# Optimization experiments

Measured on AMD Instinct MI355X. Metric: run time of the kernel, lower is better.

## Reference

```python
import jax, jax.numpy as jnp
import numpy as np

N, F_IN, E = 50000, 128, 800000
HID, HEADS, EMB = 32, 8, 64
NEG_SLOPE = 0.2


def gat_conv(x, src, dst, W_src, W_dst, att_src, att_dst, bias, heads, out_ch, concat):
    n = x.shape[0]
    h_src = (x @ W_src).reshape(n, heads, out_ch)   # [N,H,C]
    h_dst = (x @ W_dst).reshape(n, heads, out_ch)
    a_src = jnp.sum(h_src * att_src, axis=-1)       # [N,H]
    a_dst = jnp.sum(h_dst * att_dst, axis=-1)
    e = jax.nn.leaky_relu(a_src[src] + a_dst[dst], NEG_SLOPE)  # [E,H]
    # segment softmax over destination nodes (stable, max detached as in PyG)
    m = jax.ops.segment_max(e, dst, num_segments=n)
    m = jnp.where(jnp.isfinite(m), m, 0.0)
    ex = jnp.exp(e - jax.lax.stop_gradient(m)[dst])
    denom = jax.ops.segment_sum(ex, dst, num_segments=n)
    alpha = ex / (denom[dst] + 1e-16)               # [E,H]
    msg = h_src[src] * alpha[:, :, None]            # [E,H,C]
    out = jax.ops.segment_sum(msg, dst, num_segments=n)  # [N,H,C]
    if concat:
        out = out.reshape(n, heads * out_ch)
    else:
        out = out.mean(axis=1)
    return out + bias


def setup_inputs() -> dict:
    key = jax.random.key(0)
    ks = jax.random.split(key, 12)
    g = lambda k, shape: jax.random.normal(k, shape, dtype=jnp.float32) * (1.0 / np.sqrt(shape[0]))
    x = jax.random.normal(ks[0], (N, F_IN), dtype=jnp.float32)
    edge_index = jax.random.randint(ks[1], (2, E), 0, N, dtype=jnp.int64)
    return {
        "x": x,
        "edge_index": edge_index,
        "W_src1": g(ks[2], (F_IN, HEADS * HID)),
        "W_dst1": g(ks[3], (F_IN, HEADS * HID)),
        "att_src1": g(ks[4], (HEADS, HID)) * 0.1,
        "att_dst1": g(ks[5], (HEADS, HID)) * 0.1,
        "b1": jnp.zeros((HEADS * HID,), dtype=jnp.float32),
        "W_src2": g(ks[6], (HEADS * HID, EMB)),
        "W_dst2": g(ks[7], (HEADS * HID, EMB)),
        "att_src2": g(ks[8], (1, EMB)) * 0.1,
        "att_dst2": g(ks[9], (1, EMB)) * 0.1,
        "b2": jnp.zeros((EMB,), dtype=jnp.float32),
    }


def reference(x, edge_index, W_src1, W_dst1, att_src1, att_dst1, b1,
              W_src2, W_dst2, att_src2, att_dst2, b2):
    src, dst = edge_index[0], edge_index[1]
    h = gat_conv(x, src, dst, W_src1, W_dst1, att_src1, att_dst1, b1, HEADS, HID, True)
    h = jax.nn.relu(h)
    out = gat_conv(h, src, dst, W_src2, W_dst2, att_src2, att_dst2, b2, 1, EMB, False)
    return out
```

## Files before the change

kernel.cpp:

```cpp
#include <hip/hip_runtime.h>
#include <hip/hip_bf16.h>
#include <cstdint>
#include <cstddef>

#define NN    50000
#define FIN   128
#define EE    800000
#define HID_  32
#define HEADS_ 8
#define EMB_  64
#define NEG   0.2f
#define NB_SCAN 196
#define LOG2E 1.4426950408889634f

typedef short bf16x8 __attribute__((ext_vector_type(8)));
typedef float f32x4  __attribute__((ext_vector_type(4)));

static __device__ __forceinline__ ushort f2bf(float f){
    uint u = __float_as_uint(f);
    uint r = (u + 0x7FFFu + ((u >> 16) & 1u)) >> 16;
    return (ushort)r;
}
static __device__ __forceinline__ float bf2f(ushort u){
    return __uint_as_float(((uint)u) << 16);
}
static __device__ __forceinline__ float pexp(float t){
    return __builtin_amdgcn_exp2f(fmaxf(t, NEG * t));
}

__global__ __launch_bounds__(256) void k_prep(const float* __restrict__ Wsrc1, const float* __restrict__ Wdst1,
                                              const float* __restrict__ asrc1, const float* __restrict__ adst1,
                                              const float* __restrict__ Wsrc2, const float* __restrict__ Wdst2,
                                              const float* __restrict__ asrc2, const float* __restrict__ adst2,
                                              ushort* __restrict__ wt1bf, float* __restrict__ wt2,
                                              ushort* __restrict__ w1t, ushort* __restrict__ w2t){
    int idx = blockIdx.x * blockDim.x + threadIdx.x;
    if (idx < 2048){
        int f = idx >> 4, j = idx & 15;
        const float* W; const float* a; int h;
        if (j < 8) { W = Wsrc1; a = asrc1; h = j; } else { W = Wdst1; a = adst1; h = j - 8; }
        float s = 0.f;
        #pragma unroll
        for (int c = 0; c < HID_; ++c)
            s += W[(size_t)f * (HEADS_ * HID_) + h * HID_ + c] * a[h * HID_ + c];
        wt1bf[j * 128 + f] = f2bf(s * LOG2E);
    } else if (idx < 2560){
        int t = idx - 2048;
        int f = t >> 1, j = t & 1;
        const float* W = j ? Wdst2 : Wsrc2;
        const float* a = j ? adst2 : asrc2;
        float s = 0.f;
        #pragma unroll
        for (int c = 0; c < EMB_; ++c) s += W[(size_t)f * EMB_ + c] * a[c];
        wt2[j * 256 + f] = s * LOG2E;
    } else if (idx < 35328){
        int t = idx - 2560;
        int n = t >> 7, k = t & 127;
        w1t[t] = f2bf(Wsrc1[(size_t)k * 256 + n]);
    } else if (idx < 51712){
        int t = idx - 35328;
        int n = t >> 8, k = t & 255;
        w2t[t] = f2bf(Wsrc2[(size_t)k * 64 + n]);
    }
}

__global__ void k_hist(const int* __restrict__ dst, int* __restrict__ deg, int* __restrict__ rank){
    int e = blockIdx.x * blockDim.x + threadIdx.x;
    if (e < EE) rank[e] = atomicAdd(&deg[dst[e]], 1);
}

__global__ __launch_bounds__(256) void k_scanall(const int* __restrict__ deg, int* __restrict__ row_ptr,
                                                 int* __restrict__ bsum, int* __restrict__ flags){
    __shared__ int s[256];
    __shared__ int ps[256];
    int tid = threadIdx.x, b = blockIdx.x;
    int i = b * 256 + tid;
    int v = (i < NN) ? deg[i] : 0;
    s[tid] = v;
    __syncthreads();
    #pragma unroll
    for (int off = 1; off < 256; off <<= 1){
        int t = (tid >= off) ? s[tid - off] : 0;
        __syncthreads();
        s[tid] += t;
        __syncthreads();
    }
    if (tid == 255){
        bsum[b] = s[255];
        __hip_atomic_store(&flags[b], 1, __ATOMIC_RELEASE, __HIP_MEMORY_SCOPE_AGENT);
    }
    int p = 0;
    if (tid < b){
        while (__hip_atomic_load(&flags[tid], __ATOMIC_ACQUIRE, __HIP_MEMORY_SCOPE_AGENT) == 0){}
        p = bsum[tid];
    }
    ps[tid] = p;
    __syncthreads();
    #pragma unroll
    for (int off = 128; off > 0; off >>= 1){
        if (tid < off) ps[tid] += ps[tid + off];
        __syncthreads();
    }
    int boff = ps[0];
    if (i < NN) row_ptr[i] = boff + s[tid] - v;
    if (b == 0 && tid == 0) row_ptr[NN] = EE;
}

__global__ void k_scatter(const int* __restrict__ src, const int* __restrict__ dst,
                          const int* __restrict__ row_ptr, const int* __restrict__ rank,
                          int* __restrict__ col){
    int e = blockIdx.x * blockDim.x + threadIdx.x;
    if (e < EE){
        int d = dst[e];
        col[row_ptr[d] + rank[e]] = src[e];
    }
}

__global__ __launch_bounds__(256) void k_gemm1_mfma(const float* __restrict__ x,
                                                    const ushort* __restrict__ w1t,
                                                    const ushort* __restrict__ wt1bf,
                                                    ushort* __restrict__ c,
                                                    float* __restrict__ a_src1,
                                                    float* __restrict__ a_dst1){
    __shared__ ushort As[64][136];
    __shared__ ushort Bs[128][136];
    __shared__ ushort Bsa[16][136];
    const int tid = threadIdx.x;
    const int m0 = blockIdx.x * 64;
    const int n0 = blockIdx.y * 128;
    #pragma unroll
    for (int i = 0; i < 8; ++i){
        int idx = tid + i * 256;
        int r = idx >> 5, c4 = idx & 31;
        int m = m0 + r;
        float4 v = make_float4(0.f, 0.f, 0.f, 0.f);
        if (m < NN) v = *(const float4*)&x[(size_t)m * FIN + c4 * 4];
        ushort4 u; u.x = f2bf(v.x); u.y = f2bf(v.y); u.z = f2bf(v.z); u.w = f2bf(v.w);
        *(ushort4*)&As[r][c4 * 4] = u;
    }
    #pragma unroll
    for (int i = 0; i < 8; ++i){
        int idx = tid + i * 256;
        int r = idx >> 4, c8 = idx & 15;
        const ushort4* s4 = (const ushort4*)&w1t[(size_t)(n0 + r) * 128 + c8 * 8];
        *(ushort4*)&Bs[r][c8 * 8]     = s4[0];
        *(ushort4*)&Bs[r][c8 * 8 + 4] = s4[1];
    }
    if (blockIdx.y == 0){
        int r = tid >> 4, c8 = tid & 15;
        const ushort4* s4 = (const ushort4*)&wt1bf[r * 128 + c8 * 8];
        *(ushort4*)&Bsa[r][c8 * 8]     = s4[0];
        *(ushort4*)&Bsa[r][c8 * 8 + 4] = s4[1];
    }
    __syncthreads();
    const int lane = tid & 63;
    const int w    = tid >> 6;
    const int mr   = lane & 15;
    const int kg   = lane >> 4;
    f32x4 acc[8];
    #pragma unroll
    for (int i = 0; i < 8; ++i) acc[i] = (f32x4){0.f, 0.f, 0.f, 0.f};
    f32x4 acca = (f32x4){0.f, 0.f, 0.f, 0.f};
    #pragma unroll
    for (int ks = 0; ks < 4; ++ks){
        bf16x8 a = *(const bf16x8*)&As[w * 16 + mr][ks * 32 + kg * 8];
        #pragma unroll
        for (int nf = 0; nf < 8; ++nf){
            bf16x8 b = *(const bf16x8*)&Bs[nf * 16 + mr][ks * 32 + kg * 8];
            acc[nf] = __builtin_amdgcn_mfma_f32_16x16x32_bf16(a, b, acc[nf], 0, 0, 0);
        }
        if (blockIdx.y == 0){
            bf16x8 ba = *(const bf16x8*)&Bsa[mr][ks * 32 + kg * 8];
            acca = __builtin_amdgcn_mfma_f32_16x16x32_bf16(a, ba, acca, 0, 0, 0);
        }
    }
    #pragma unroll
    for (int nf = 0; nf < 8; ++nf){
        int colb = n0 + nf * 16 + mr;
        #pragma unroll
        for (int r = 0; r < 4; ++r){
            int row = m0 + w * 16 + kg * 4 + r;
            if (row < NN) c[(size_t)row * 256 + colb] = f2bf(acc[nf][r]);
        }
    }
    if (blockIdx.y == 0){
        int j = mr;
        #pragma unroll
        for (int r = 0; r < 4; ++r){
            int row = m0 + w * 16 + kg * 4 + r;
            if (row < NN){
                if (j < 8) a_src1[(size_t)row * 8 + j]       = acca[r];
                else       a_dst1[(size_t)row * 8 + (j - 8)] = acca[r];
            }
        }
    }
}

__global__ __launch_bounds__(256) void k_gemm2_mfma(const ushort* __restrict__ hbf,
                                                    const ushort* __restrict__ w2t,
                                                    ushort* __restrict__ c2){
    __shared__ ushort As[64][264];
    __shared__ ushort Bs[64][264];
    const int tid = threadIdx.x;
    const int m0 = blockIdx.x * 64;
    #pragma unroll
    for (int i = 0; i < 8; ++i){
        int idx = tid + i * 256;
        int r = idx >> 5, c8 = idx & 31;
        int m = m0 + r;
        ushort4 v0 = make_ushort4(0,0,0,0), v1 = make_ushort4(0,0,0,0);
        if (m < NN){
            const ushort4* s4 = (const ushort4*)&hbf[(size_t)m * 256 + c8 * 8];
            v0 = s4[0]; v1 = s4[1];
        }
        *(ushort4*)&As[r][c8 * 8]     = v0;
        *(ushort4*)&As[r][c8 * 8 + 4] = v1;
    }
    #pragma unroll
    for (int i = 0; i < 8; ++i){
        int idx = tid + i * 256;
        int r = idx >> 5, c8 = idx & 31;
        const ushort4* s4 = (const ushort4*)&w2t[(size_t)r * 256 + c8 * 8];
        *(ushort4*)&Bs[r][c8 * 8]     = s4[0];
        *(ushort4*)&Bs[r][c8 * 8 + 4] = s4[1];
    }
    __syncthreads();
    const int lane = tid & 63;
    const int w    = tid >> 6;
    const int mr   = lane & 15;
    const int kg   = lane >> 4;
    f32x4 acc[4];
    #pragma unroll
    for (int i = 0; i < 4; ++i) acc[i] = (f32x4){0.f, 0.f, 0.f, 0.f};
    #pragma unroll
    for (int ks = 0; ks < 8; ++ks){
        bf16x8 a = *(const bf16x8*)&As[w * 16 + mr][ks * 32 + kg * 8];
        #pragma unroll
        for (int nf = 0; nf < 4; ++nf){
            bf16x8 b = *(const bf16x8*)&Bs[nf * 16 + mr][ks * 32 + kg * 8];
            acc[nf] = __builtin_amdgcn_mfma_f32_16x16x32_bf16(a, b, acc[nf], 0, 0, 0);
        }
    }
    #pragma unroll
    for (int nf = 0; nf < 4; ++nf){
        int colb = nf * 16 + mr;
        #pragma unroll
        for (int r = 0; r < 4; ++r){
            int row = m0 + w * 16 + kg * 4 + r;
            if (row < NN) c2[(size_t)row * 64 + colb] = f2bf(acc[nf][r]);
        }
    }
}

__global__ __launch_bounds__(256) void k_agg1(const ushort* __restrict__ hsrc, const float* __restrict__ a_src,
                                              const float* __restrict__ a_dst, const int* __restrict__ row_ptr,
                                              const int* __restrict__ col, const float* __restrict__ b1,
                                              const float* __restrict__ wt2,
                                              ushort* __restrict__ hout_bf,
                                              float* __restrict__ a_src2, float* __restrict__ a_dst2){
    int node = blockIdx.x * 4 + (threadIdx.x >> 6);
    if (node >= NN) return;
    int lane = threadIdx.x & 63;
    int head = lane >> 3;
    float ad = a_dst[(size_t)node * 8 + head];
    const ushort4* h4 = (const ushort4*)hsrc;
    float4 acc = make_float4(0.f, 0.f, 0.f, 0.f);
    float den = 0.f;
    int b = row_ptr[node], en = row_ptr[node + 1];
    int i = b;
    for (; i + 8 <= en; i += 8){
        int ss[8]; float e[8]; ushort4 v[8]; float p[8];
        #pragma unroll
        for (int j = 0; j < 8; ++j) ss[j] = col[i + j];
        #pragma unroll
        for (int j = 0; j < 8; ++j) e[j] = a_src[(size_t)ss[j] * 8 + head];
        #pragma unroll
        for (int j = 0; j < 8; ++j) v[j] = h4[(size_t)ss[j] * 64 + lane];
        #pragma unroll
        for (int j = 0; j < 8; ++j) p[j] = pexp(e[j] + ad);
        #pragma unroll
        for (int j = 0; j < 8; ++j){
            acc.x += p[j] * bf2f(v[j].x);
            acc.y += p[j] * bf2f(v[j].y);
            acc.z += p[j] * bf2f(v[j].z);
            acc.w += p[j] * bf2f(v[j].w);
            den += p[j];
        }
    }
    for (; i < en; ++i){
        int s = col[i];
        float p = pexp(a_src[(size_t)s * 8 + head] + ad);
        ushort4 v = h4[(size_t)s * 64 + lane];
        acc.x += p * bf2f(v.x); acc.y += p * bf2f(v.y);
        acc.z += p * bf2f(v.z); acc.w += p * bf2f(v.w);
        den += p;
    }
    float inv = 1.f / (den + 1e-16f);
    float4 bb = ((const float4*)b1)[lane];
    float4 o;
    o.x = fmaxf(acc.x * inv + bb.x, 0.f);
    o.y = fmaxf(acc.y * inv + bb.y, 0.f);
    o.z = fmaxf(acc.z * inv + bb.z, 0.f);
    o.w = fmaxf(acc.w * inv + bb.w, 0.f);
    ushort4 ob; ob.x = f2bf(o.x); ob.y = f2bf(o.y); ob.z = f2bf(o.z); ob.w = f2bf(o.w);
    ((ushort4*)hout_bf)[(size_t)node * 64 + lane] = ob;
    float4 ws4 = ((const float4*)wt2)[lane];
    float4 wd4 = ((const float4*)(wt2 + 256))[lane];
    float ss2 = o.x*ws4.x + o.y*ws4.y + o.z*ws4.z + o.w*ws4.w;
    float sd2 = o.x*wd4.x + o.y*wd4.y + o.z*wd4.z + o.w*wd4.w;
    #pragma unroll
    for (int off = 32; off > 0; off >>= 1){
        ss2 += __shfl_xor(ss2, off);
        sd2 += __shfl_xor(sd2, off);
    }
    if (lane == 0){ a_src2[node] = ss2; a_dst2[node] = sd2; }
}

__global__ __launch_bounds__(256) void k_agg2(const ushort* __restrict__ h2bf, const float* __restrict__ a_src2,
                                              const float* __restrict__ a_dst2, const int* __restrict__ row_ptr,
                                              const int* __restrict__ col, const float* __restrict__ b2,
                                              float* __restrict__ out){
    int node = blockIdx.x * 4 + (threadIdx.x >> 6);
    if (node >= NN) return;
    int lane = threadIdx.x & 63;
    float ad = a_dst2[node];
    float acc = 0.f, den = 0.f;
    int b = row_ptr[node], en = row_ptr[node + 1];
    int i = b;
    for (; i + 8 <= en; i += 8){
        int ss[8]; float e[8]; ushort u[8]; float p[8];
        #pragma unroll
        for (int j = 0; j < 8; ++j) ss[j] = col[i + j];
        #pragma unroll
        for (int j = 0; j < 8; ++j) e[j] = a_src2[ss[j]];
        #pragma unroll
        for (int j = 0; j < 8; ++j) u[j] = h2bf[(size_t)ss[j] * 64 + lane];
        #pragma unroll
        for (int j = 0; j < 8; ++j) p[j] = pexp(e[j] + ad);
        #pragma unroll
        for (int j = 0; j < 8; ++j){
            acc += p[j] * bf2f(u[j]);
            den += p[j];
        }
    }
    for (; i < en; ++i){
        int s = col[i];
        float p = pexp(a_src2[s] + ad);
        acc += p * bf2f(h2bf[(size_t)s * 64 + lane]);
        den += p;
    }
    out[(size_t)node * 64 + lane] = acc / (den + 1e-16f) + b2[lane];
}

extern "C" void kernel_launch(void* const* d_in, const int* in_sizes, int n_in,
                              void* d_out, int out_size, void* d_ws, size_t ws_size,
                              hipStream_t stream){
    const float* x        = (const float*)d_in[0];
    const int*   ei       = (const int*)  d_in[1];
    const float* Wsrc1    = (const float*)d_in[2];
    const float* Wdst1    = (const float*)d_in[3];
    const float* att_src1 = (const float*)d_in[4];
    const float* att_dst1 = (const float*)d_in[5];
    const float* b1       = (const float*)d_in[6];
    const float* Wsrc2    = (const float*)d_in[7];
    const float* Wdst2    = (const float*)d_in[8];
    const float* att_src2 = (const float*)d_in[9];
    const float* att_dst2 = (const float*)d_in[10];
    const float* b2       = (const float*)d_in[11];
    float* out = (float*)d_out;
    const int* srcp = ei;
    const int* dstp = ei + EE;

    char* base = (char*)d_ws;
    ushort* hbf1   = (ushort*)base;  base += (size_t)NN * 256 * 2;
    ushort* hrel   = (ushort*)base;  base += (size_t)NN * 256 * 2;
    ushort* h2bf   = (ushort*)base;  base += (size_t)NN * 64 * 2;
    float*  a_src1 = (float*)base;   base += (size_t)NN * 8 * 4;
    float*  a_dst1 = (float*)base;   base += (size_t)NN * 8 * 4;
    float*  a_src2 = (float*)base;   base += (size_t)NN * 4;
    float*  a_dst2 = (float*)base;   base += (size_t)NN * 4;
    ushort* wt1bf  = (ushort*)base;  base += 2048 * 2;
    float*  wt2    = (float*)base;   base += 512 * 4;
    ushort* w1t    = (ushort*)base;  base += 32768 * 2;
    ushort* w2t    = (ushort*)base;  base += 16384 * 2;
    int* deg     = (int*)base;       base += (size_t)NN * 4;
    int* flags   = (int*)base;       base += 256 * 4;
    int* row_ptr = (int*)base;       base += (size_t)(NN + 1) * 4;
    int* rank    = (int*)base;       base += (size_t)EE * 4;
    int* col     = (int*)base;       base += (size_t)EE * 4;
    int* bsum    = (int*)base;       base += 256 * 4;

    hipMemsetAsync(deg, 0, (NN + 256) * sizeof(int), stream);

    k_prep<<<202, 256, 0, stream>>>(Wsrc1, Wdst1, att_src1, att_dst1,
                                    Wsrc2, Wdst2, att_src2, att_dst2,
                                    wt1bf, wt2, w1t, w2t);

    k_hist<<<(EE + 255) / 256, 256, 0, stream>>>(dstp, deg, rank);
    k_scanall<<<NB_SCAN, 256, 0, stream>>>(deg, row_ptr, bsum, flags);
    k_scatter<<<(EE + 255) / 256, 256, 0, stream>>>(srcp, dstp, row_ptr, rank, col);

    dim3 g1((NN + 63) / 64, 2);
    k_gemm1_mfma<<<g1, 256, 0, stream>>>(x, w1t, wt1bf, hbf1, a_src1, a_dst1);

    k_agg1<<<(NN + 3) / 4, 256, 0, stream>>>(hbf1, a_src1, a_dst1, row_ptr, col, b1, wt2,
                                             hrel, a_src2, a_dst2);

    k_gemm2_mfma<<<(NN + 63) / 64, 256, 0, stream>>>(hrel, w2t, h2bf);

    k_agg2<<<(NN + 3) / 4, 256, 0, stream>>>(h2bf, a_src2, a_dst2, row_ptr, col, b2, out);
}
```

Before: 217.2 us.

## Split node features into per-head 32-channel planes for cache-local gathers

Stores layer-1 and layer-2 features as head-major planes of 32 bf16 channels per node. The aggregation kernels become head-sliced: each block handles one plane, with four edges processed in parallel per wavefront and combined by shuffles. The second-layer attention scalars are accumulated atomically across heads and zeroed by an extended memset. The aim is to keep each plane's gather working set small enough for cache reuse, in exchange for eight times as many blocks, repeated row_ptr and col reads per head, and float atomics.

```diff
diff --git a/kernel.cpp b/kernel.cpp
--- a/kernel.cpp
+++ b/kernel.cpp
@@ -180,7 +180,8 @@
         #pragma unroll
         for (int r = 0; r < 4; ++r){
             int row = m0 + w * 16 + kg * 4 + r;
-            if (row < NN) c[(size_t)row * 256 + colb] = f2bf(acc[nf][r]);
+            if (row < NN)
+                c[((size_t)(colb >> 5) * NN + row) * 32 + (colb & 31)] = f2bf(acc[nf][r]);
         }
     }
     if (blockIdx.y == 0){
@@ -210,7 +211,7 @@
         int m = m0 + r;
         ushort4 v0 = make_ushort4(0,0,0,0), v1 = make_ushort4(0,0,0,0);
         if (m < NN){
-            const ushort4* s4 = (const ushort4*)&hbf[(size_t)m * 256 + c8 * 8];
+            const ushort4* s4 = (const ushort4*)&hbf[((size_t)(c8 >> 2) * NN + m) * 32 + (c8 & 3) * 8];
             v0 = s4[0]; v1 = s4[1];
         }
         *(ushort4*)&As[r][c8 * 8]     = v0;
@@ -247,109 +248,123 @@
         #pragma unroll
         for (int r = 0; r < 4; ++r){
             int row = m0 + w * 16 + kg * 4 + r;
-            if (row < NN) c2[(size_t)row * 64 + colb] = f2bf(acc[nf][r]);
-        }
-    }
-}
-
-__global__ __launch_bounds__(256) void k_agg1(const ushort* __restrict__ hsrc, const float* __restrict__ a_src,
-                                              const float* __restrict__ a_dst, const int* __restrict__ row_ptr,
-                                              const int* __restrict__ col, const float* __restrict__ b1,
-                                              const float* __restrict__ wt2,
-                                              ushort* __restrict__ hout_bf,
-                                              float* __restrict__ a_src2, float* __restrict__ a_dst2){
-    int node = blockIdx.x * 4 + (threadIdx.x >> 6);
+            if (row < NN)
+                c2[((size_t)(colb >> 5) * NN + row) * 32 + (colb & 31)] = f2bf(acc[nf][r]);
+        }
+    }
+}
+
+__global__ __launch_bounds__(256) void k_agg1_s(const ushort* __restrict__ hb1s,
+                                                const float* __restrict__ a_src, const float* __restrict__ a_dst,
+                                                const int* __restrict__ row_ptr, const int* __restrict__ col,
+                                                const float* __restrict__ b1, const float* __restrict__ wt2,
+                                                ushort* __restrict__ hrels,
+                                                float* __restrict__ a_src2, float* __restrict__ a_dst2){
+    const int p = blockIdx.x & 7;
+    const int node = (blockIdx.x >> 3) * 4 + (threadIdx.x >> 6);
     if (node >= NN) return;
-    int lane = threadIdx.x & 63;
-    int head = lane >> 3;
-    float ad = a_dst[(size_t)node * 8 + head];
-    const ushort4* h4 = (const ushort4*)hsrc;
-    float4 acc = make_float4(0.f, 0.f, 0.f, 0.f);
-    float den = 0.f;
-    int b = row_ptr[node], en = row_ptr[node + 1];
+    const int lane = threadIdx.x & 63;
+    const int slot = lane >> 4;
+    const int c2 = lane & 15;
+    const ushort* hp = hb1s + (size_t)p * NN * 32;
+    const float ad = a_dst[(size_t)node * 8 + p];
+    float acc0 = 0.f, acc1 = 0.f, den = 0.f;
+    const int b = row_ptr[node], en = row_ptr[node + 1];
     int i = b;
     for (; i + 8 <= en; i += 8){
-        int ss[8]; float e[8]; ushort4 v[8]; float p[8];
-        #pragma unroll
-        for (int j = 0; j < 8; ++j) ss[j] = col[i + j];
-        #pragma unroll
-        for (int j = 0; j < 8; ++j) e[j] = a_src[(size_t)ss[j] * 8 + head];
-        #pragma unroll
-        for (int j = 0; j < 8; ++j) v[j] = h4[(size_t)ss[j] * 64 + lane];
-        #pragma unroll
-        for (int j = 0; j < 8; ++j) p[j] = pexp(e[j] + ad);
-        #pragma unroll
-        for (int j = 0; j < 8; ++j){
-            acc.x += p[j] * bf2f(v[j].x);
-            acc.y += p[j] * bf2f(v[j].y);
-            acc.z += p[j] * bf2f(v[j].z);
-            acc.w += p[j] * bf2f(v[j].w);
-            den += p[j];
-        }
-    }
-    for (; i < en; ++i){
-        int s = col[i];
-        float p = pexp(a_src[(size_t)s * 8 + head] + ad);
-        ushort4 v = h4[(size_t)s * 64 + lane];
-        acc.x += p * bf2f(v.x); acc.y += p * bf2f(v.y);
-        acc.z += p * bf2f(v.z); acc.w += p * bf2f(v.w);
-        den += p;
-    }
+        int iA = i + slot, iB = i + 4 + slot;
+        int sA = col[iA], sB = col[iB];
+        float eA = a_src[(size_t)sA * 8 + p];
+        float eB = a_src[(size_t)sB * 8 + p];
+        uint uA = *(const uint*)&hp[(size_t)sA * 32 + c2 * 2];
+        uint uB = *(const uint*)&hp[(size_t)sB * 32 + c2 * 2];
+        float pA = pexp(eA + ad), pB = pexp(eB + ad);
+        acc0 += pA * bf2f((ushort)(uA & 0xffff)) + pB * bf2f((ushort)(uB & 0xffff));
+        acc1 += pA * bf2f((ushort)(uA >> 16))    + pB * bf2f((ushort)(uB >> 16));
+        den  += pA + pB;
+    }
+    for (; i < en; i += 4){
+        int idx = i + slot;
+        int s = col[idx < en ? idx : en - 1];
+        float e = a_src[(size_t)s * 8 + p];
+        uint u = *(const uint*)&hp[(size_t)s * 32 + c2 * 2];
+        float pv = (idx < en) ? pexp(e + ad) : 0.f;
+        acc0 += pv * bf2f((ushort)(u & 0xffff));
+        acc1 += pv * bf2f((ushort)(u >> 16));
+        den  += pv;
+    }
+    acc0 += __shfl_xor(acc0, 16); acc0 += __shfl_xor(acc0, 32);
+    acc1 += __shfl_xor(acc1, 16); acc1 += __shfl_xor(acc1, 32);
+    den  += __shfl_xor(den , 16); den  += __shfl_xor(den , 32);
     float inv = 1.f / (den + 1e-16f);
-    float4 bb = ((const float4*)b1)[lane];
-    float4 o;
-    o.x = fmaxf(acc.x * inv + bb.x, 0.f);
-    o.y = fmaxf(acc.y * inv + bb.y, 0.f);
-    o.z = fmaxf(acc.z * inv + bb.z, 0.f);
-    o.w = fmaxf(acc.w * inv + bb.w, 0.f);
-    ushort4 ob; ob.x = f2bf(o.x); ob.y = f2bf(o.y); ob.z = f2bf(o.z); ob.w = f2bf(o.w);
-    ((ushort4*)hout_bf)[(size_t)node * 64 + lane] = ob;
-    float4 ws4 = ((const float4*)wt2)[lane];
-    float4 wd4 = ((const float4*)(wt2 + 256))[lane];
-    float ss2 = o.x*ws4.x + o.y*ws4.y + o.z*ws4.z + o.w*ws4.w;
-    float sd2 = o.x*wd4.x + o.y*wd4.y + o.z*wd4.z + o.w*wd4.w;
-    #pragma unroll
-    for (int off = 32; off > 0; off >>= 1){
-        ss2 += __shfl_xor(ss2, off);
-        sd2 += __shfl_xor(sd2, off);
-    }
-    if (lane == 0){ a_src2[node] = ss2; a_dst2[node] = sd2; }
-}
-
-__global__ __launch_bounds__(256) void k_agg2(const ushort* __restrict__ h2bf, const float* __restrict__ a_src2,
-                                              const float* __restrict__ a_dst2, const int* __restrict__ row_ptr,
-                                              const int* __restrict__ col, const float* __restrict__ b2,
-                                              float* __restrict__ out){
-    int node = blockIdx.x * 4 + (threadIdx.x >> 6);
+    int ch = p * 32 + c2 * 2;
+    float o0 = fmaxf(acc0 * inv + b1[ch],     0.f);
+    float o1 = fmaxf(acc1 * inv + b1[ch + 1], 0.f);
+    float ps = o0 * wt2[ch]       + o1 * wt2[ch + 1];
+    float pd = o0 * wt2[256 + ch] + o1 * wt2[256 + ch + 1];
+    #pragma unroll
+    for (int off = 1; off < 16; off <<= 1){
+        ps += __shfl_xor(ps, off);
+        pd += __shfl_xor(pd, off);
+    }
+    if (lane == 0){
+        atomicAdd(&a_src2[node], ps);
+        atomicAdd(&a_dst2[node], pd);
+    }
+    if (lane < 16){
+        ushort2 ob; ob.x = f2bf(o0); ob.y = f2bf(o1);
+        *(ushort2*)&hrels[((size_t)p * NN + node) * 32 + c2 * 2] = ob;
+    }
+}
+
+__global__ __launch_bounds__(256) void k_agg2_s(const ushort* __restrict__ h2s,
+                                                const float* __restrict__ a_src2, const float* __restrict__ a_dst2,
+                                                const int* __restrict__ row_ptr, const int* __restrict__ col,
+                                                const float* __restrict__ b2, float* __restrict__ out){
+    const int q = blockIdx.x & 7;
+    const int p = q >> 2;
+    const int node = ((blockIdx.x >> 3) * 4 + (q & 3)) * 4 + (threadIdx.x >> 6);
     if (node >= NN) return;
-    int lane = threadIdx.x & 63;
-    float ad = a_dst2[node];
-    float acc = 0.f, den = 0.f;
-    int b = row_ptr[node], en = row_ptr[node + 1];
+    const int lane = threadIdx.x & 63;
+    const int slot = lane >> 4;
+    const int c2 = lane & 15;
+    const ushort* hp = h2s + (size_t)p * NN * 32;
+    const float ad = a_dst2[node];
+    float acc0 = 0.f, acc1 = 0.f, den = 0.f;
+    const int b = row_ptr[node], en = row_ptr[node + 1];
     int i = b;
     for (; i + 8 <= en; i += 8){
-        int ss[8]; float e[8]; ushort u[8]; float p[8];
-        #pragma unroll
-        for (int j = 0; j < 8; ++j) ss[j] = col[i + j];
-        #pragma unroll
-        for (int j = 0; j < 8; ++j) e[j] = a_src2[ss[j]];
-        #pragma unroll
-        for (int j = 0; j < 8; ++j) u[j] = h2bf[(size_t)ss[j] * 64 + lane];
-        #pragma unroll
-        for (int j = 0; j < 8; ++j) p[j] = pexp(e[j] + ad);
-        #pragma unroll
-        for (int j = 0; j < 8; ++j){
-            acc += p[j] * bf2f(u[j]);
-            den += p[j];
-        }
-    }
-    for (; i < en; ++i){
-        int s = col[i];
-        float p = pexp(a_src2[s] + ad);
-        acc += p * bf2f(h2bf[(size_t)s * 64 + lane]);
-        den += p;
-    }
-    out[(size_t)node * 64 + lane] = acc / (den + 1e-16f) + b2[lane];
+        int iA = i + slot, iB = i + 4 + slot;
+        int sA = col[iA], sB = col[iB];
+        float eA = a_src2[sA], eB = a_src2[sB];
+        uint uA = *(const uint*)&hp[(size_t)sA * 32 + c2 * 2];
+        uint uB = *(const uint*)&hp[(size_t)sB * 32 + c2 * 2];
+        float pA = pexp(eA + ad), pB = pexp(eB + ad);
+        acc0 += pA * bf2f((ushort)(uA & 0xffff)) + pB * bf2f((ushort)(uB & 0xffff));
+        acc1 += pA * bf2f((ushort)(uA >> 16))    + pB * bf2f((ushort)(uB >> 16));
+        den  += pA + pB;
+    }
+    for (; i < en; i += 4){
+        int idx = i + slot;
+        int s = col[idx < en ? idx : en - 1];
+        float e = a_src2[s];
+        uint u = *(const uint*)&hp[(size_t)s * 32 + c2 * 2];
+        float pv = (idx < en) ? pexp(e + ad) : 0.f;
+        acc0 += pv * bf2f((ushort)(u & 0xffff));
+        acc1 += pv * bf2f((ushort)(u >> 16));
+        den  += pv;
+    }
+    acc0 += __shfl_xor(acc0, 16); acc0 += __shfl_xor(acc0, 32);
+    acc1 += __shfl_xor(acc1, 16); acc1 += __shfl_xor(acc1, 32);
+    den  += __shfl_xor(den , 16); den  += __shfl_xor(den , 32);
+    float inv = 1.f / (den + 1e-16f);
+    if (lane < 16){
+        int ch = p * 32 + c2 * 2;
+        float2 o;
+        o.x = acc0 * inv + b2[ch];
+        o.y = acc1 * inv + b2[ch + 1];
+        *(float2*)&out[(size_t)node * 64 + ch] = o;
+    }
 }
 
 extern "C" void kernel_launch(void* const* d_in, const int* in_sizes, int n_in,
@@ -372,25 +387,25 @@
     const int* dstp = ei + EE;
 
     char* base = (char*)d_ws;
-    ushort* hbf1   = (ushort*)base;  base += (size_t)NN * 256 * 2;
-    ushort* hrel   = (ushort*)base;  base += (size_t)NN * 256 * 2;
-    ushort* h2bf   = (ushort*)base;  base += (size_t)NN * 64 * 2;
+    ushort* hb1s   = (ushort*)base;  base += (size_t)NN * 256 * 2;
+    ushort* hrels  = (ushort*)base;  base += (size_t)NN * 256 * 2;
+    ushort* h2s    = (ushort*)base;  base += (size_t)NN * 64 * 2;
     float*  a_src1 = (float*)base;   base += (size_t)NN * 8 * 4;
     float*  a_dst1 = (float*)base;   base += (size_t)NN * 8 * 4;
-    float*  a_src2 = (float*)base;   base += (size_t)NN * 4;
-    float*  a_dst2 = (float*)base;   base += (size_t)NN * 4;
     ushort* wt1bf  = (ushort*)base;  base += 2048 * 2;
     float*  wt2    = (float*)base;   base += 512 * 4;
     ushort* w1t    = (ushort*)base;  base += 32768 * 2;
     ushort* w2t    = (ushort*)base;  base += 16384 * 2;
-    int* deg     = (int*)base;       base += (size_t)NN * 4;
-    int* flags   = (int*)base;       base += 256 * 4;
+    int*   deg     = (int*)base;     base += (size_t)NN * 4;
+    int*   flags   = (int*)base;     base += 256 * 4;
+    float* a_src2  = (float*)base;   base += (size_t)NN * 4;
+    float* a_dst2  = (float*)base;   base += (size_t)NN * 4;
     int* row_ptr = (int*)base;       base += (size_t)(NN + 1) * 4;
     int* rank    = (int*)base;       base += (size_t)EE * 4;
     int* col     = (int*)base;       base += (size_t)EE * 4;
     int* bsum    = (int*)base;       base += 256 * 4;
 
-    hipMemsetAsync(deg, 0, (NN + 256) * sizeof(int), stream);
+    (void)hipMemsetAsync(deg, 0, (size_t)(NN + 256 + 2 * NN) * sizeof(int), stream);
 
     k_prep<<<202, 256, 0, stream>>>(Wsrc1, Wdst1, att_src1, att_dst1,
                                     Wsrc2, Wdst2, att_src2, att_dst2,
@@ -401,12 +416,12 @@
     k_scatter<<<(EE + 255) / 256, 256, 0, stream>>>(srcp, dstp, row_ptr, rank, col);
 
     dim3 g1((NN + 63) / 64, 2);
-    k_gemm1_mfma<<<g1, 256, 0, stream>>>(x, w1t, wt1bf, hbf1, a_src1, a_dst1);
-
-    k_agg1<<<(NN + 3) / 4, 256, 0, stream>>>(hbf1, a_src1, a_dst1, row_ptr, col, b1, wt2,
-                                             hrel, a_src2, a_dst2);
-
-    k_gemm2_mfma<<<(NN + 63) / 64, 256, 0, stream>>>(hrel, w2t, h2bf);
-
-    k_agg2<<<(NN + 3) / 4, 256, 0, stream>>>(h2bf, a_src2, a_dst2, row_ptr, col, b2, out);
-}
+    k_gemm1_mfma<<<g1, 256, 0, stream>>>(x, w1t, wt1bf, hb1s, a_src1, a_dst1);
+
+    k_agg1_s<<<12500 * 8, 256, 0, stream>>>(hb1s, a_src1, a_dst1, row_ptr, col, b1, wt2,
+                                            hrels, a_src2, a_dst2);
+
+    k_gemm2_mfma<<<(NN + 63) / 64, 256, 0, stream>>>(hrels, w2t, h2s);
+
+    k_agg2_s<<<3125 * 8, 256, 0, stream>>>(h2s, a_src2, a_dst2, row_ptr, col, b2, out);
+}
```

New measurement: 354.1 us. +63.0%, slower.

## Merge prep with histogram and GEMM1 with CSR scatter; shrink aggregation unroll

Applied to the files above, without the earlier changes.

Independent kernels are merged by block-index partitioning: weight prep and the degree histogram share one launch, and the CSR scatter runs as extra blocks of the first GEMM kernel. This removes two launches and lets independent work overlap on the device. The aggregation loops also drop from an 8-edge to a 4-edge unroll with tree-summed partial products, which lowers register pressure but leaves fewer loads in flight per wave. The GEMM grid is flattened to 1D.

```diff
diff --git a/kernel.cpp b/kernel.cpp
--- a/kernel.cpp
+++ b/kernel.cpp
@@ -11,6 +11,9 @@
 #define EMB_  64
 #define NEG   0.2f
 #define NB_SCAN 196
+#define NB_PREP 202
+#define NB_EDGE 3125
+#define NB_GEMM1 1564
 #define LOG2E 1.4426950408889634f
 
 typedef short bf16x8 __attribute__((ext_vector_type(8)));
@@ -28,12 +31,19 @@
     return __builtin_amdgcn_exp2f(fmaxf(t, NEG * t));
 }
 
-__global__ __launch_bounds__(256) void k_prep(const float* __restrict__ Wsrc1, const float* __restrict__ Wdst1,
-                                              const float* __restrict__ asrc1, const float* __restrict__ adst1,
-                                              const float* __restrict__ Wsrc2, const float* __restrict__ Wdst2,
-                                              const float* __restrict__ asrc2, const float* __restrict__ adst2,
-                                              ushort* __restrict__ wt1bf, float* __restrict__ wt2,
-                                              ushort* __restrict__ w1t, ushort* __restrict__ w2t){
+__global__ __launch_bounds__(256) void k_prep_hist(const float* __restrict__ Wsrc1, const float* __restrict__ Wdst1,
+                                                   const float* __restrict__ asrc1, const float* __restrict__ adst1,
+                                                   const float* __restrict__ Wsrc2, const float* __restrict__ Wdst2,
+                                                   const float* __restrict__ asrc2, const float* __restrict__ adst2,
+                                                   ushort* __restrict__ wt1bf, float* __restrict__ wt2,
+                                                   ushort* __restrict__ w1t, ushort* __restrict__ w2t,
+                                                   const int* __restrict__ dst, int* __restrict__ deg,
+                                                   int* __restrict__ rank){
+    if (blockIdx.x >= NB_PREP){
+        int e = (blockIdx.x - NB_PREP) * 256 + threadIdx.x;
+        if (e < EE) rank[e] = atomicAdd(&deg[dst[e]], 1);
+        return;
+    }
     int idx = blockIdx.x * blockDim.x + threadIdx.x;
     if (idx < 2048){
         int f = idx >> 4, j = idx & 15;
@@ -64,11 +74,6 @@
     }
 }
 
-__global__ void k_hist(const int* __restrict__ dst, int* __restrict__ deg, int* __restrict__ rank){
-    int e = blockIdx.x * blockDim.x + threadIdx.x;
-    if (e < EE) rank[e] = atomicAdd(&deg[dst[e]], 1);
-}
-
 __global__ __launch_bounds__(256) void k_scanall(const int* __restrict__ deg, int* __restrict__ row_ptr,
                                                  int* __restrict__ bsum, int* __restrict__ flags){
     __shared__ int s[256];
@@ -106,28 +111,29 @@
     if (b == 0 && tid == 0) row_ptr[NN] = EE;
 }
 
-__global__ void k_scatter(const int* __restrict__ src, const int* __restrict__ dst,
-                          const int* __restrict__ row_ptr, const int* __restrict__ rank,
-                          int* __restrict__ col){
-    int e = blockIdx.x * blockDim.x + threadIdx.x;
-    if (e < EE){
-        int d = dst[e];
-        col[row_ptr[d] + rank[e]] = src[e];
-    }
-}
-
-__global__ __launch_bounds__(256) void k_gemm1_mfma(const float* __restrict__ x,
-                                                    const ushort* __restrict__ w1t,
-                                                    const ushort* __restrict__ wt1bf,
-                                                    ushort* __restrict__ c,
-                                                    float* __restrict__ a_src1,
-                                                    float* __restrict__ a_dst1){
+__global__ __launch_bounds__(256) void k_gemm1_scatter(const float* __restrict__ x,
+                                                       const ushort* __restrict__ w1t,
+                                                       const ushort* __restrict__ wt1bf,
+                                                       ushort* __restrict__ c,
+                                                       float* __restrict__ a_src1,
+                                                       float* __restrict__ a_dst1,
+                                                       const int* __restrict__ src, const int* __restrict__ dstp,
+                                                       const int* __restrict__ row_ptr, const int* __restrict__ rank,
+                                                       int* __restrict__ col){
     __shared__ ushort As[64][136];
     __shared__ ushort Bs[128][136];
     __shared__ ushort Bsa[16][136];
+    if (blockIdx.x >= NB_GEMM1){
+        int e = (blockIdx.x - NB_GEMM1) * 256 + threadIdx.x;
+        if (e < EE){
+            int d = dstp[e];
+            col[row_ptr[d] + rank[e]] = src[e];
+        }
+        return;
+    }
     const int tid = threadIdx.x;
-    const int m0 = blockIdx.x * 64;
-    const int n0 = blockIdx.y * 128;
+    const int m0 = (blockIdx.x >> 1) * 64;
+    const int n0 = (blockIdx.x & 1) * 128;
     #pragma unroll
     for (int i = 0; i < 8; ++i){
         int idx = tid + i * 256;
@@ -146,7 +152,7 @@
         *(ushort4*)&Bs[r][c8 * 8]     = s4[0];
         *(ushort4*)&Bs[r][c8 * 8 + 4] = s4[1];
     }
-    if (blockIdx.y == 0){
+    if (n0 == 0){
         int r = tid >> 4, c8 = tid & 15;
         const ushort4* s4 = (const ushort4*)&wt1bf[r * 128 + c8 * 8];
         *(ushort4*)&Bsa[r][c8 * 8]     = s4[0];
@@ -169,7 +175,7 @@
             bf16x8 b = *(const bf16x8*)&Bs[nf * 16 + mr][ks * 32 + kg * 8];
             acc[nf] = __builtin_amdgcn_mfma_f32_16x16x32_bf16(a, b, acc[nf], 0, 0, 0);
         }
-        if (blockIdx.y == 0){
+        if (n0 == 0){
             bf16x8 ba = *(const bf16x8*)&Bsa[mr][ks * 32 + kg * 8];
             acca = __builtin_amdgcn_mfma_f32_16x16x32_bf16(a, ba, acca, 0, 0, 0);
         }
@@ -183,7 +189,7 @@
             if (row < NN) c[(size_t)row * 256 + colb] = f2bf(acc[nf][r]);
         }
     }
-    if (blockIdx.y == 0){
+    if (n0 == 0){
         int j = mr;
         #pragma unroll
         for (int r = 0; r < 4; ++r){
@@ -268,24 +274,25 @@
     float den = 0.f;
     int b = row_ptr[node], en = row_ptr[node + 1];
     int i = b;
-    for (; i + 8 <= en; i += 8){
-        int ss[8]; float e[8]; ushort4 v[8]; float p[8];
-        #pragma unroll
-        for (int j = 0; j < 8; ++j) ss[j] = col[i + j];
-        #pragma unroll
-        for (int j = 0; j < 8; ++j) e[j] = a_src[(size_t)ss[j] * 8 + head];
-        #pragma unroll
-        for (int j = 0; j < 8; ++j) v[j] = h4[(size_t)ss[j] * 64 + lane];
-        #pragma unroll
-        for (int j = 0; j < 8; ++j) p[j] = pexp(e[j] + ad);
-        #pragma unroll
-        for (int j = 0; j < 8; ++j){
-            acc.x += p[j] * bf2f(v[j].x);
-            acc.y += p[j] * bf2f(v[j].y);
-            acc.z += p[j] * bf2f(v[j].z);
-            acc.w += p[j] * bf2f(v[j].w);
-            den += p[j];
-        }
+    for (; i + 4 <= en; i += 4){
+        int s0 = col[i], s1 = col[i+1], s2 = col[i+2], s3 = col[i+3];
+        float e0 = a_src[(size_t)s0 * 8 + head];
+        float e1 = a_src[(size_t)s1 * 8 + head];
+        float e2 = a_src[(size_t)s2 * 8 + head];
+        float e3 = a_src[(size_t)s3 * 8 + head];
+        ushort4 v0 = h4[(size_t)s0 * 64 + lane];
+        ushort4 v1 = h4[(size_t)s1 * 64 + lane];
+        ushort4 v2 = h4[(size_t)s2 * 64 + lane];
+        ushort4 v3 = h4[(size_t)s3 * 64 + lane];
+        float p0 = pexp(e0 + ad);
+        float p1 = pexp(e1 + ad);
+        float p2 = pexp(e2 + ad);
+        float p3 = pexp(e3 + ad);
+        acc.x += p0*bf2f(v0.x) + p1*bf2f(v1.x) + p2*bf2f(v2.x) + p3*bf2f(v3.x);
+        acc.y += p0*bf2f(v0.y) + p1*bf2f(v1.y) + p2*bf2f(v2.y) + p3*bf2f(v3.y);
+        acc.z += p0*bf2f(v0.z) + p1*bf2f(v1.z) + p2*bf2f(v2.z) + p3*bf2f(v3.z);
+        acc.w += p0*bf2f(v0.w) + p1*bf2f(v1.w) + p2*bf2f(v2.w) + p3*bf2f(v3.w);
+        den += p0 + p1 + p2 + p3;
     }
     for (; i < en; ++i){
         int s = col[i];
@@ -327,21 +334,19 @@
     float acc = 0.f, den = 0.f;
     int b = row_ptr[node], en = row_ptr[node + 1];
     int i = b;
-    for (; i + 8 <= en; i += 8){
-        int ss[8]; float e[8]; ushort u[8]; float p[8];
-        #pragma unroll
-        for (int j = 0; j < 8; ++j) ss[j] = col[i + j];
-        #pragma unroll
-        for (int j = 0; j < 8; ++j) e[j] = a_src2[ss[j]];
-        #pragma unroll
-        for (int j = 0; j < 8; ++j) u[j] = h2bf[(size_t)ss[j] * 64 + lane];
-        #pragma unroll
-        for (int j = 0; j < 8; ++j) p[j] = pexp(e[j] + ad);
-        #pragma unroll
-        for (int j = 0; j < 8; ++j){
-            acc += p[j] * bf2f(u[j]);
-            den += p[j];
-        }
+    for (; i + 4 <= en; i += 4){
+        int s0 = col[i], s1 = col[i+1], s2 = col[i+2], s3 = col[i+3];
+        float e0 = a_src2[s0], e1 = a_src2[s1], e2 = a_src2[s2], e3 = a_src2[s3];
+        ushort u0 = h2bf[(size_t)s0 * 64 + lane];
+        ushort u1 = h2bf[(size_t)s1 * 64 + lane];
+        ushort u2 = h2bf[(size_t)s2 * 64 + lane];
+        ushort u3 = h2bf[(size_t)s3 * 64 + lane];
+        float p0 = pexp(e0 + ad);
+        float p1 = pexp(e1 + ad);
+        float p2 = pexp(e2 + ad);
+        float p3 = pexp(e3 + ad);
+        acc += p0*bf2f(u0) + p1*bf2f(u1) + p2*bf2f(u2) + p3*bf2f(u3);
+        den += p0 + p1 + p2 + p3;
     }
     for (; i < en; ++i){
         int s = col[i];
@@ -390,23 +395,17 @@
     int* col     = (int*)base;       base += (size_t)EE * 4;
     int* bsum    = (int*)base;       base += 256 * 4;
 
-    hipMemsetAsync(deg, 0, (NN + 256) * sizeof(int), stream);
-
-    k_prep<<<202, 256, 0, stream>>>(Wsrc1, Wdst1, att_src1, att_dst1,
-                                    Wsrc2, Wdst2, att_src2, att_dst2,
-                                    wt1bf, wt2, w1t, w2t);
-
-    k_hist<<<(EE + 255) / 256, 256, 0, stream>>>(dstp, deg, rank);
+    (void)hipMemsetAsync(deg, 0, (NN + 256) * sizeof(int), stream);
+
+    k_prep_hist<<<NB_PREP + NB_EDGE, 256, 0, stream>>>(Wsrc1, Wdst1, att_src1, att_dst1,
+                                                       Wsrc2, Wdst2, att_src2, att_dst2,
+                                                       wt1bf, wt2, w1t, w2t,
+                                                       dstp, deg, rank);
     k_scanall<<<NB_SCAN, 256, 0, stream>>>(deg, row_ptr, bsum, flags);
-    k_scatter<<<(EE + 255) / 256, 256, 0, stream>>>(srcp, dstp, row_ptr, rank, col);
-
-    dim3 g1((NN + 63) / 64, 2);
-    k_gemm1_mfma<<<g1, 256, 0, stream>>>(x, w1t, wt1bf, hbf1, a_src1, a_dst1);
-
+    k_gemm1_scatter<<<NB_GEMM1 + NB_EDGE, 256, 0, stream>>>(x, w1t, wt1bf, hbf1, a_src1, a_dst1,
+                                                            srcp, dstp, row_ptr, rank, col);
     k_agg1<<<(NN + 3) / 4, 256, 0, stream>>>(hbf1, a_src1, a_dst1, row_ptr, col, b1, wt2,
                                              hrel, a_src2, a_dst2);
-
     k_gemm2_mfma<<<(NN + 63) / 64, 256, 0, stream>>>(hrel, w2t, h2bf);
-
     k_agg2<<<(NN + 3) / 4, 256, 0, stream>>>(h2bf, a_src2, a_dst2, row_ptr, col, b2, out);
 }
```

New measurement: 202.7 us. 1.07x faster.
